# Performance work log

Measured on AMD Instinct MI355X. Metric: run time of the kernel, lower is better.

The kernel has to match this reference:

```python
import jax, jax.numpy as jnp
import numpy as np

K_NEIGHBORS = 32
BN_EPS = 1e-5


def setup_inputs() -> dict:
    key = jax.random.key(0)
    ks = jax.random.split(key, 5)
    B, N, C, OUT = 16, 2048, 3, 32
    x = jax.random.normal(ks[0], (B, N, C), dtype=jnp.float32)
    W1 = jax.random.normal(ks[1], (2 * C, 2 * C), dtype=jnp.float32) * 0.3
    b1 = jax.random.normal(ks[2], (2 * C,), dtype=jnp.float32) * 0.05
    W2 = jax.random.normal(ks[3], (2 * C, OUT), dtype=jnp.float32) * 0.3
    b2 = jax.random.normal(ks[4], (OUT,), dtype=jnp.float32) * 0.05
    return {
        "x": x,
        "W1": W1, "b1": b1,
        "gamma1": jnp.ones((2 * C,), jnp.float32), "beta1": jnp.zeros((2 * C,), jnp.float32),
        "W2": W2, "b2": b2,
        "gamma2": jnp.ones((OUT,), jnp.float32), "beta2": jnp.zeros((OUT,), jnp.float32),
    }


def _batchnorm_train(h, gamma, beta):
    # normalize over all axes except the last (channel) axis, biased variance
    axes = tuple(range(h.ndim - 1))
    mean = jnp.mean(h, axis=axes)
    var = jnp.var(h, axis=axes)
    return gamma * (h - mean) * jax.lax.rsqrt(var + BN_EPS) + beta


def reference(x, W1, b1, gamma1, beta1, W2, b2, gamma2, beta2):
    B, N, C = x.shape
    K = min(K_NEIGHBORS, N)
    # brute-force KNN: squared euclidean distances [B,N,N]
    sq = jnp.sum(x * x, axis=-1)
    d = sq[:, :, None] + sq[:, None, :] - 2.0 * jnp.einsum('bnc,bmc->bnm', x, x)
    _, idx = jax.lax.top_k(-d, K)  # [B,N,K] nearest (self first)
    # gather neighbor points: [B,N,K,C]
    knn = jax.vmap(lambda pts, i: pts[i])(x, idx)
    diffs = x[:, :, None, :] - knn
    h = jnp.concatenate([jnp.broadcast_to(x[:, :, None, :], (B, N, K, C)), diffs], axis=-1)  # [B,N,K,2C]
    h = jax.nn.elu(_batchnorm_train(h @ W1 + b1, gamma1, beta1))
    h = jnp.max(h, axis=2)  # max-pool over K neighbors -> [B,N,2C]
    y = jax.nn.elu(_batchnorm_train(h @ W2 + b2, gamma2, beta2))
    return y
```

## Files before the change

kernel.cpp:

```cpp
#include <hip/hip_runtime.h>
#include <math.h>

namespace {
constexpr int NB = 16, NP = 2048, KNN = 32, CH1 = 6, CH2 = 32;
constexpr int QPB = 8;
constexpr int NBLK = NB * NP / QPB;
constexpr float BN_EPS = 1e-5f;

constexpr size_t OFF_S1REP   = 0;
constexpr size_t OFF_STATS2L = 768;
constexpr size_t OFF_SC1     = 1664;
constexpr size_t OFF_P       = 2048;
constexpr size_t OFF_MINQ    = OFF_P + sizeof(float)*NB*NP*CH1;
}

typedef __attribute__((ext_vector_type(2))) float f32x2;

__device__ __forceinline__ f32x2 pk_mul(f32x2 a, f32x2 b) {
  f32x2 d; asm("v_pk_mul_f32 %0, %1, %2" : "=v"(d) : "v"(a), "v"(b)); return d;
}
__device__ __forceinline__ f32x2 pk_add(f32x2 a, f32x2 b) {
  f32x2 d; asm("v_pk_add_f32 %0, %1, %2" : "=v"(d) : "v"(a), "v"(b)); return d;
}

template <int C> __device__ __forceinline__ int dpp0i(int x) {
  return __builtin_amdgcn_update_dpp(0, x, C, 0xf, 0xf, true);
}
template <int C> __device__ __forceinline__ float dpp0f(float x) {
  return __uint_as_float((unsigned)__builtin_amdgcn_update_dpp(
      0, (int)__float_as_uint(x), C, 0xf, 0xf, true));
}
template <int C> __device__ __forceinline__ float dppInff(float x) {
  return __uint_as_float((unsigned)__builtin_amdgcn_update_dpp(
      0x7F800000, (int)__float_as_uint(x), C, 0xf, 0xf, false));
}
__device__ __forceinline__ int wave_isum_bcast(int x) {
  x += dpp0i<0x111>(x); x += dpp0i<0x112>(x); x += dpp0i<0x114>(x);
  x += dpp0i<0x118>(x); x += dpp0i<0x142>(x); x += dpp0i<0x143>(x);
  return __builtin_amdgcn_readlane(x, 63);
}
__device__ __forceinline__ float wave_fsum63(float x) {
  x += dpp0f<0x111>(x); x += dpp0f<0x112>(x); x += dpp0f<0x114>(x);
  x += dpp0f<0x118>(x); x += dpp0f<0x142>(x); x += dpp0f<0x143>(x);
  return x;
}
__device__ __forceinline__ float wave_fmin63(float x) {
  x = fminf(x, dppInff<0x111>(x)); x = fminf(x, dppInff<0x112>(x));
  x = fminf(x, dppInff<0x114>(x)); x = fminf(x, dppInff<0x118>(x));
  x = fminf(x, dppInff<0x142>(x)); x = fminf(x, dppInff<0x143>(x));
  return x;
}

#define BSEL(m, x, y) ((((x)) & (m)) | (((y)) & ~(m)))

__global__ __launch_bounds__(512, 6) void knn_kernel(const float* __restrict__ x,
                                                     const float* __restrict__ W1,
                                                     const float* __restrict__ b1,
                                                     float* __restrict__ pout,
                                                     float* __restrict__ minq,
                                                     double* __restrict__ s1rep) {
  __shared__ float4 XC[512], YC[512], ZC[512], WC[512];
  __shared__ float red[12][QPB];
  const int lane = threadIdx.x & 63;
  const int w    = threadIdx.x >> 6;
  const int qi   = blockIdx.x * QPB + w;
  const int b    = qi >> 11;
  const int n    = qi & (NP - 1);

  const float* xb = x + (size_t)b * NP * 3;
  {
    const int t = threadIdx.x;
    const int g0 = t >> 6, ls = t & 63;
    float xx[4], yy[4], zz[4], ww[4];
#pragma unroll
    for (int k = 0; k < 4; ++k) {
      const float* pp = xb + (g0*256 + k*64 + ls) * 3;
      float a0 = pp[0], a1 = pp[1], a2 = pp[2];
      xx[k] = a0; yy[k] = a1; zz[k] = a2;
      ww[k] = __fadd_rn(__fadd_rn(__fmul_rn(a0,a0), __fmul_rn(a1,a1)), __fmul_rn(a2,a2));
    }
    XC[t] = (float4){xx[0], xx[1], xx[2], xx[3]};
    YC[t] = (float4){yy[0], yy[1], yy[2], yy[3]};
    ZC[t] = (float4){zz[0], zz[1], zz[2], zz[3]};
    WC[t] = (float4){ww[0], ww[1], ww[2], ww[3]};
  }
  __syncthreads();

  const float* Xs = (const float*)XC;
  const float* Ys = (const float*)YC;
  const float* Zs = (const float*)ZC;
  const float* Ws = (const float*)WC;

  const int vq = n >> 6, lq = n & 63;
  const int qidx = (((vq >> 2) << 6) | lq) * 4 + (vq & 3);
  const float qx = Xs[qidx], qy = Ys[qidx], qz = Zs[qidx], qw = Ws[qidx];
  const f32x2 qx2 = {qx,qx}, qy2 = {qy,qy}, qz2 = {qz,qz}, qw2 = {qw,qw};

  unsigned dd[32];
#pragma unroll
  for (int g = 0; g < 8; ++g) {
    const int cs = g*64 + lane;
    float4 X = XC[cs], Y = YC[cs], Z = ZC[cs], Wv = WC[cs];
    f32x2 x01 = {X.x,X.y}, y01 = {Y.x,Y.y}, z01 = {Z.x,Z.y}, w01 = {Wv.x,Wv.y};
    f32x2 x23 = {X.z,X.w}, y23 = {Y.z,Y.w}, z23 = {Z.z,Z.w}, w23 = {Wv.z,Wv.w};
    f32x2 dotA = pk_add(pk_add(pk_mul(qx2,x01), pk_mul(qy2,y01)), pk_mul(qz2,z01));
    f32x2 dotB = pk_add(pk_add(pk_mul(qx2,x23), pk_mul(qy2,y23)), pk_mul(qz2,z23));
    f32x2 ssA = pk_add(qw2, w01), ssB = pk_add(qw2, w23);
    f32x2 dA = pk_add(dotA, dotA), dB = pk_add(dotB, dotB);
    dd[31-(4*g+0)] = __float_as_uint(__fsub_rn(ssA.x, dA.x));
    dd[31-(4*g+1)] = __float_as_uint(__fsub_rn(ssA.y, dA.y));
    dd[31-(4*g+2)] = __float_as_uint(__fsub_rn(ssB.x, dB.x));
    dd[31-(4*g+3)] = __float_as_uint(__fsub_rn(ssB.y, dB.y));
  }

  unsigned h[16], l[16];
#pragma unroll
  for (int g = 0; g < 16; ++g) {
    h[g] = __builtin_amdgcn_perm(dd[g], dd[g+16], 0x07060302u);
    l[g] = __builtin_amdgcn_perm(dd[g], dd[g+16], 0x05040100u);
  }
#pragma unroll
  for (int g = 0; g < 8; ++g) {
    unsigned hi = h[g], lo = h[g+8];
    h[g]   = __builtin_amdgcn_perm(hi, lo, 0x07030501u);
    h[g+8] = __builtin_amdgcn_perm(hi, lo, 0x06020400u);
  }
#pragma unroll
  for (int g = 0; g < 8; ++g) {
    int k = (g >> 2)*8 + (g & 3);
    unsigned A = h[k], B = h[k+4];
    h[k]   = BSEL(0x0F0F0F0Fu, B >> 4, A);
    h[k+4] = BSEL(0xF0F0F0F0u, A << 4, B);
  }
#pragma unroll
  for (int g = 0; g < 8; ++g) {
    int k = (g >> 1)*4 + (g & 1);
    unsigned A = h[k], B = h[k+2];
    h[k]   = BSEL(0x33333333u, B >> 2, A);
    h[k+2] = BSEL(0xCCCCCCCCu, A << 2, B);
  }
#pragma unroll
  for (int g = 0; g < 8; ++g) {
    int k = g*2;
    unsigned A = h[k], B = h[k+1];
    h[k]   = BSEL(0x55555555u, B >> 1, A);
    h[k+1] = BSEL(0xAAAAAAAAu, A << 1, B);
  }

  unsigned alive = 0xFFFFFFFFu, below = 0u;
  int rem = KNN, ca = 2048;
#pragma unroll
  for (int i = 1; i <= 6; ++i) {
    unsigned zeros = BSEL(h[i], 0u, alive);
    int c0 = wave_isum_bcast(__popc(zeros));
    if (c0 >= rem) { alive = zeros; ca = c0; }
    else { rem -= c0; below |= zeros; alive &= h[i]; ca -= c0; }
  }
#pragma unroll
  for (int i = 7; i <= 15; ++i) {
    if (ca != rem) {
      unsigned zeros = BSEL(h[i], 0u, alive);
      int c0 = wave_isum_bcast(__popc(zeros));
      if (c0 >= rem) { alive = zeros; ca = c0; }
      else { rem -= c0; below |= zeros; alive &= h[i]; ca -= c0; }
    }
  }
  unsigned sel;
  if (__builtin_expect(ca == rem, 1)) {
    sel = below | alive;
  } else {
#pragma unroll
    for (int g = 0; g < 8; ++g) {
      unsigned hi = l[g], lo = l[g+8];
      l[g]   = __builtin_amdgcn_perm(hi, lo, 0x07030501u);
      l[g+8] = __builtin_amdgcn_perm(hi, lo, 0x06020400u);
    }
#pragma unroll
    for (int g = 0; g < 8; ++g) {
      int k = (g >> 2)*8 + (g & 3);
      unsigned A = l[k], B = l[k+4];
      l[k]   = BSEL(0x0F0F0F0Fu, B >> 4, A);
      l[k+4] = BSEL(0xF0F0F0F0u, A << 4, B);
    }
#pragma unroll
    for (int g = 0; g < 8; ++g) {
      int k = (g >> 1)*4 + (g & 1);
      unsigned A = l[k], B = l[k+2];
      l[k]   = BSEL(0x33333333u, B >> 2, A);
      l[k+2] = BSEL(0xCCCCCCCCu, A << 2, B);
    }
#pragma unroll
    for (int g = 0; g < 8; ++g) {
      int k = g*2;
      unsigned A = l[k], B = l[k+1];
      l[k]   = BSEL(0x55555555u, B >> 1, A);
      l[k+1] = BSEL(0xAAAAAAAAu, A << 1, B);
    }
#pragma unroll
    for (int i = 0; i < 16; ++i) {
      if (ca != rem) {
        unsigned zeros = BSEL(l[i], 0u, alive);
        int c0 = wave_isum_bcast(__popc(zeros));
        if (c0 >= rem) { alive = zeros; ca = c0; }
        else { rem -= c0; below |= zeros; alive &= l[i]; ca -= c0; }
      }
    }
    sel = below;
    if (ca == rem) {
      sel |= alive;
    } else {
      for (int v = 0; v < 32; ++v) {
        if (rem <= 0) break;
        bool mine = (alive >> v) & 1;
        unsigned long long mb = __ballot(mine);
        int c = __popcll(mb);
        if (c <= rem) { if (mine) sel |= 1u << v; rem -= c; }
        else {
          if (mine && (int)__popcll(mb & ((1ull << lane) - 1)) < rem) sel |= 1u << v;
          rem = 0;
        }
      }
    }
  }

  float w3[CH1], w4[CH1], w5[CH1];
#pragma unroll
  for (int c = 0; c < CH1; ++c) { w3[c]=W1[3*CH1+c]; w4[c]=W1[4*CH1+c]; w5[c]=W1[5*CH1+c]; }
  float sq_[CH1], sqq[CH1], mn[CH1];
#pragma unroll
  for (int c = 0; c < CH1; ++c) { sq_[c] = 0.f; sqq[c] = 0.f; mn[c] = INFINITY; }
  unsigned m = sel;
  while (m) {
    int v = __builtin_ctz(m); m &= m - 1;
    int idx = (((v >> 2) << 6) | lane) * 4 + (v & 3);
    float px_ = Xs[idx], py_ = Ys[idx], pz_ = Zs[idx];
#pragma unroll
    for (int c = 0; c < CH1; ++c) {
      float qv = px_*w3[c] + py_*w4[c] + pz_*w5[c];
      sq_[c] += qv; sqq[c] += qv*qv; mn[c] = fminf(mn[c], qv);
    }
  }

  float pv[CH1];
#pragma unroll
  for (int c = 0; c < CH1; ++c) {
    float qv = qx*w3[c] + qy*w4[c] + qz*w5[c];
    pv[c] = b1[c] + qx*W1[c] + qy*W1[CH1+c] + qz*W1[2*CH1+c] + qv;
  }

#pragma unroll
  for (int c = 0; c < CH1; ++c) {
    float s  = wave_fsum63(sq_[c]);
    float s2 = wave_fsum63(sqq[c]);
    float mm = wave_fmin63(mn[c]);
    if (lane == 63) {
      minq[qi*CH1 + c] = mm;
      red[c][w]       = fmaf(32.f, pv[c], -s);
      red[CH1 + c][w] = fmaf(32.f, pv[c]*pv[c], fmaf(-2.f*pv[c], s, s2));
    }
  }
  if (lane == 0) {
#pragma unroll
    for (int c = 0; c < CH1; ++c) pout[qi*CH1 + c] = pv[c];
  }
  __syncthreads();
  if (threadIdx.x < 12) {
    float s = 0.f;
#pragma unroll
    for (int ww2 = 0; ww2 < QPB; ++ww2) s += red[threadIdx.x][ww2];
    atomicAdd(s1rep + (blockIdx.x & 7) * 12 + threadIdx.x, (double)s);
  }
}

__global__ __launch_bounds__(256) void stage2_kernel(const float* __restrict__ p,
                                                     const float* __restrict__ minq,
                                                     const double* __restrict__ s1rep,
                                                     const float* __restrict__ gamma1,
                                                     const float* __restrict__ beta1,
                                                     float* __restrict__ sc1g,
                                                     double* __restrict__ stats2L) {
  __shared__ double tot1[12];
  __shared__ float sc1s[12];
  __shared__ float acc[4][27];
  const int t = threadIdx.x;
  if (t < 12) {
    double s = 0.0;
#pragma unroll
    for (int r = 0; r < 8; ++r) s += s1rep[r*12 + t];
    tot1[t] = s;
  }
  __syncthreads();
  if (t < CH1) {
    double cnt  = (double)NB * NP * KNN;
    double mean = tot1[t] / cnt;
    double var  = tot1[CH1 + t] / cnt - mean * mean;
    float scale = gamma1[t] / sqrtf((float)var + BN_EPS);
    sc1s[t] = scale; sc1s[CH1 + t] = beta1[t] - (float)mean * scale;
  }
  __syncthreads();
  if (blockIdx.x == 0 && t < 12) sc1g[t] = sc1s[t];

  const int qi = blockIdx.x * 256 + t;
  const int w = t >> 6, lane = t & 63;
  float me[CH1];
#pragma unroll
  for (int c = 0; c < CH1; ++c) {
    float v = fmaf(sc1s[c], p[qi*CH1 + c] - minq[qi*CH1 + c], sc1s[CH1 + c]);
    me[c] = v > 0.f ? v : expm1f(v);
  }
  float vals[27];
#pragma unroll
  for (int c = 0; c < CH1; ++c) vals[c] = me[c];
  {
    int id = 6;
#pragma unroll
    for (int c = 0; c < CH1; ++c)
#pragma unroll
      for (int d = c; d < CH1; ++d) { vals[id] = me[c]*me[d]; ++id; }
  }
#pragma unroll
  for (int k = 0; k < 27; ++k) {
    float s = wave_fsum63(vals[k]);
    if (lane == 63) acc[w][k] = s;
  }
  __syncthreads();
  if (t < 27)
    atomicAdd(stats2L + (blockIdx.x & 3) * 27 + t,
              (double)((acc[0][t] + acc[1][t]) + (acc[2][t] + acc[3][t])));
}

__global__ __launch_bounds__(256) void out_kernel(const float* __restrict__ p,
                                                  const float* __restrict__ minq,
                                                  const float* __restrict__ sc1,
                                                  const float* __restrict__ W2,
                                                  const float* __restrict__ b2,
                                                  const double* __restrict__ stats2L,
                                                  const float* __restrict__ gamma2,
                                                  const float* __restrict__ beta2,
                                                  float* __restrict__ out) {
  __shared__ float m2[27];
  __shared__ float me_lds[8][CH1];
  __shared__ float s2s[CH2], s2h[CH2];
  const int t = threadIdx.x;
  if (t < 27)
    m2[t] = (float)(((stats2L[t] + stats2L[27+t]) + (stats2L[54+t] + stats2L[81+t])));
  const int qbase = blockIdx.x * 8;
  if (t >= 64 && t < 112) {
    int qs = (t - 64) / 6, c = (t - 64) % 6;
    int qi = qbase + qs;
    float v = fmaf(sc1[c], p[qi*CH1 + c] - minq[qi*CH1 + c], sc1[CH1 + c]);
    me_lds[qs][c] = v > 0.f ? v : expm1f(v);
  }
  __syncthreads();
  if (t < CH2) {
    float wv[CH1];
#pragma unroll
    for (int c = 0; c < CH1; ++c) wv[c] = W2[c*CH2 + t];
    float sy = 0.f;
#pragma unroll
    for (int c = 0; c < CH1; ++c) sy = fmaf(wv[c], m2[c], sy);
    float sy2 = 0.f;
    {
      int id = 6;
#pragma unroll
      for (int c = 0; c < CH1; ++c)
#pragma unroll
        for (int d = c; d < CH1; ++d) {
          float coef = (c == d) ? wv[c]*wv[c] : 2.f*wv[c]*wv[d];
          sy2 = fmaf(coef, m2[id], sy2); ++id;
        }
    }
    const double N = (double)NB * NP;
    double bo   = (double)b2[t];
    double mean = ((double)sy + N*bo) / N;
    double Ey2  = ((double)sy2 + 2.0*bo*(double)sy + N*bo*bo) / N;
    double var  = Ey2 - mean*mean;
    float scale = gamma2[t] / sqrtf((float)var + BN_EPS);
    s2s[t] = scale; s2h[t] = beta2[t] - (float)mean * scale;
  }
  __syncthreads();
  const int qs = t >> 5, o = t & 31;
  const int qi = qbase + qs;
  float y = b2[o];
#pragma unroll
  for (int c = 0; c < CH1; ++c) y = fmaf(me_lds[qs][c], W2[c*CH2 + o], y);
  float r = fmaf(s2s[o], y, s2h[o]);
  out[(size_t)qi*CH2 + o] = r > 0.f ? r : expm1f(r);
}

extern "C" void kernel_launch(void* const* d_in, const int* in_sizes, int n_in,
                              void* d_out, int out_size, void* d_ws, size_t ws_size,
                              hipStream_t stream) {
  const float* x      = (const float*)d_in[0];
  const float* W1     = (const float*)d_in[1];
  const float* b1     = (const float*)d_in[2];
  const float* gamma1 = (const float*)d_in[3];
  const float* beta1  = (const float*)d_in[4];
  const float* W2     = (const float*)d_in[5];
  const float* b2     = (const float*)d_in[6];
  const float* gamma2 = (const float*)d_in[7];
  const float* beta2  = (const float*)d_in[8];
  float* out = (float*)d_out;
  char* ws = (char*)d_ws;

  double* s1rep   = (double*)(ws + OFF_S1REP);
  double* stats2L = (double*)(ws + OFF_STATS2L);
  float* sc1  = (float*)(ws + OFF_SC1);
  float* p    = (float*)(ws + OFF_P);
  float* minq = (float*)(ws + OFF_MINQ);

  hipMemsetAsync(ws, 0, 1664, stream);

  knn_kernel   <<<dim3(NBLK),       dim3(512), 0, stream>>>(x, W1, b1, p, minq, s1rep);
  stage2_kernel<<<dim3(NB*NP/256),  dim3(256), 0, stream>>>(p, minq, s1rep, gamma1, beta1,
                                                            sc1, stats2L);
  out_kernel   <<<dim3(NB*NP/8),    dim3(256), 0, stream>>>(p, minq, sc1, W2, b2,
                                                            stats2L, gamma2, beta2, out);
}
```

Baseline: 72.04 us.

## Process two queries per wave in KNN kernel to amortize tile loads

```diff
diff --git a/kernel.cpp b/kernel.cpp
--- a/kernel.cpp
+++ b/kernel.cpp
@@ -3,7 +3,7 @@
 
 namespace {
 constexpr int NB = 16, NP = 2048, KNN = 32, CH1 = 6, CH2 = 32;
-constexpr int QPB = 8;
+constexpr int QPB = 16;
 constexpr int NBLK = NB * NP / QPB;
 constexpr float BN_EPS = 1e-5f;
 
@@ -53,19 +53,69 @@
 
 #define BSEL(m, x, y) ((((x)) & (m)) | (((y)) & ~(m)))
 
-__global__ __launch_bounds__(512, 6) void knn_kernel(const float* __restrict__ x,
+#define RROUND(alive, below, rem, ca, plane)                  \
+  { unsigned z_ = (alive) & ~(plane);                         \
+    int c_ = wave_isum_bcast(__popc(z_));                     \
+    bool t_ = (c_ >= (rem));                                  \
+    below = t_ ? (below) : ((below) | z_);                    \
+    alive = t_ ? z_ : ((alive) & (plane));                    \
+    ca    = t_ ? c_ : (ca) - c_;                              \
+    rem   = t_ ? (rem) : (rem) - c_; }
+
+#define J16_SPLIT(dd, h, l)                                          \
+  _Pragma("unroll") for (int g_ = 0; g_ < 16; ++g_) {                \
+    h[g_] = __builtin_amdgcn_perm(dd[g_], dd[g_+16], 0x07060302u);   \
+    l[g_] = __builtin_amdgcn_perm(dd[g_], dd[g_+16], 0x05040100u); }
+
+#define TR16(a)                                                      \
+  _Pragma("unroll") for (int g_ = 0; g_ < 8; ++g_) {                 \
+    unsigned hi_ = a[g_], lo_ = a[g_+8];                             \
+    a[g_]   = __builtin_amdgcn_perm(hi_, lo_, 0x07030501u);          \
+    a[g_+8] = __builtin_amdgcn_perm(hi_, lo_, 0x06020400u); }        \
+  _Pragma("unroll") for (int g_ = 0; g_ < 8; ++g_) {                 \
+    int k_ = (g_ >> 2)*8 + (g_ & 3);                                 \
+    unsigned A_ = a[k_], B_ = a[k_+4];                               \
+    a[k_]   = BSEL(0x0F0F0F0Fu, B_ >> 4, A_);                        \
+    a[k_+4] = BSEL(0xF0F0F0F0u, A_ << 4, B_); }                      \
+  _Pragma("unroll") for (int g_ = 0; g_ < 8; ++g_) {                 \
+    int k_ = (g_ >> 1)*4 + (g_ & 1);                                 \
+    unsigned A_ = a[k_], B_ = a[k_+2];                               \
+    a[k_]   = BSEL(0x33333333u, B_ >> 2, A_);                        \
+    a[k_+2] = BSEL(0xCCCCCCCCu, A_ << 2, B_); }                      \
+  _Pragma("unroll") for (int g_ = 0; g_ < 8; ++g_) {                 \
+    int k_ = g_*2;                                                   \
+    unsigned A_ = a[k_], B_ = a[k_+1];                               \
+    a[k_]   = BSEL(0x55555555u, B_ >> 1, A_);                        \
+    a[k_+1] = BSEL(0xAAAAAAAAu, A_ << 1, B_); }
+
+#define TIEBREAK(alive, sel, rem)                                    \
+  for (int v_ = 0; v_ < 32; ++v_) {                                  \
+    if ((rem) <= 0) break;                                           \
+    bool mine_ = ((alive) >> v_) & 1;                                \
+    unsigned long long mb_ = __ballot(mine_);                        \
+    int c_ = __popcll(mb_);                                          \
+    if (c_ <= (rem)) { if (mine_) (sel) |= 1u << v_; (rem) -= c_; }  \
+    else {                                                           \
+      if (mine_ && (int)__popcll(mb_ & ((1ull << lane) - 1)) < (rem))\
+        (sel) |= 1u << v_;                                           \
+      (rem) = 0;                                                     \
+    }                                                                \
+  }
+
+__global__ __launch_bounds__(512, 4) void knn_kernel(const float* __restrict__ x,
                                                      const float* __restrict__ W1,
                                                      const float* __restrict__ b1,
                                                      float* __restrict__ pout,
                                                      float* __restrict__ minq,
                                                      double* __restrict__ s1rep) {
   __shared__ float4 XC[512], YC[512], ZC[512], WC[512];
-  __shared__ float red[12][QPB];
+  __shared__ float red[12][8];
   const int lane = threadIdx.x & 63;
   const int w    = threadIdx.x >> 6;
-  const int qi   = blockIdx.x * QPB + w;
-  const int b    = qi >> 11;
-  const int n    = qi & (NP - 1);
+  const int qiA  = blockIdx.x * QPB + w * 2;
+  const int qiB  = qiA + 1;
+  const int b    = qiA >> 11;
+  const int nA   = qiA & (NP - 1), nB = qiB & (NP - 1);
 
   const float* xb = x + (size_t)b * NP * 3;
   {
@@ -91,145 +141,94 @@
   const float* Zs = (const float*)ZC;
   const float* Ws = (const float*)WC;
 
-  const int vq = n >> 6, lq = n & 63;
-  const int qidx = (((vq >> 2) << 6) | lq) * 4 + (vq & 3);
-  const float qx = Xs[qidx], qy = Ys[qidx], qz = Zs[qidx], qw = Ws[qidx];
-  const f32x2 qx2 = {qx,qx}, qy2 = {qy,qy}, qz2 = {qz,qz}, qw2 = {qw,qw};
-
-  unsigned dd[32];
+  const int vqA = nA >> 6, lqA = nA & 63;
+  const int qidxA = (((vqA >> 2) << 6) | lqA) * 4 + (vqA & 3);
+  const float qxA = Xs[qidxA], qyA = Ys[qidxA], qzA = Zs[qidxA], qwA = Ws[qidxA];
+  const int vqB = nB >> 6, lqB = nB & 63;
+  const int qidxB = (((vqB >> 2) << 6) | lqB) * 4 + (vqB & 3);
+  const float qxB = Xs[qidxB], qyB = Ys[qidxB], qzB = Zs[qidxB], qwB = Ws[qidxB];
+  const f32x2 qxA2 = {qxA,qxA}, qyA2 = {qyA,qyA}, qzA2 = {qzA,qzA}, qwA2 = {qwA,qwA};
+  const f32x2 qxB2 = {qxB,qxB}, qyB2 = {qyB,qyB}, qzB2 = {qzB,qzB}, qwB2 = {qwB,qwB};
+
+  unsigned dA[32], dB[32];
 #pragma unroll
   for (int g = 0; g < 8; ++g) {
     const int cs = g*64 + lane;
     float4 X = XC[cs], Y = YC[cs], Z = ZC[cs], Wv = WC[cs];
     f32x2 x01 = {X.x,X.y}, y01 = {Y.x,Y.y}, z01 = {Z.x,Z.y}, w01 = {Wv.x,Wv.y};
     f32x2 x23 = {X.z,X.w}, y23 = {Y.z,Y.w}, z23 = {Z.z,Z.w}, w23 = {Wv.z,Wv.w};
-    f32x2 dotA = pk_add(pk_add(pk_mul(qx2,x01), pk_mul(qy2,y01)), pk_mul(qz2,z01));
-    f32x2 dotB = pk_add(pk_add(pk_mul(qx2,x23), pk_mul(qy2,y23)), pk_mul(qz2,z23));
-    f32x2 ssA = pk_add(qw2, w01), ssB = pk_add(qw2, w23);
-    f32x2 dA = pk_add(dotA, dotA), dB = pk_add(dotB, dotB);
-    dd[31-(4*g+0)] = __float_as_uint(__fsub_rn(ssA.x, dA.x));
-    dd[31-(4*g+1)] = __float_as_uint(__fsub_rn(ssA.y, dA.y));
-    dd[31-(4*g+2)] = __float_as_uint(__fsub_rn(ssB.x, dB.x));
-    dd[31-(4*g+3)] = __float_as_uint(__fsub_rn(ssB.y, dB.y));
-  }
-
-  unsigned h[16], l[16];
-#pragma unroll
-  for (int g = 0; g < 16; ++g) {
-    h[g] = __builtin_amdgcn_perm(dd[g], dd[g+16], 0x07060302u);
-    l[g] = __builtin_amdgcn_perm(dd[g], dd[g+16], 0x05040100u);
-  }
-#pragma unroll
-  for (int g = 0; g < 8; ++g) {
-    unsigned hi = h[g], lo = h[g+8];
-    h[g]   = __builtin_amdgcn_perm(hi, lo, 0x07030501u);
-    h[g+8] = __builtin_amdgcn_perm(hi, lo, 0x06020400u);
-  }
-#pragma unroll
-  for (int g = 0; g < 8; ++g) {
-    int k = (g >> 2)*8 + (g & 3);
-    unsigned A = h[k], B = h[k+4];
-    h[k]   = BSEL(0x0F0F0F0Fu, B >> 4, A);
-    h[k+4] = BSEL(0xF0F0F0F0u, A << 4, B);
-  }
-#pragma unroll
-  for (int g = 0; g < 8; ++g) {
-    int k = (g >> 1)*4 + (g & 1);
-    unsigned A = h[k], B = h[k+2];
-    h[k]   = BSEL(0x33333333u, B >> 2, A);
-    h[k+2] = BSEL(0xCCCCCCCCu, A << 2, B);
-  }
-#pragma unroll
-  for (int g = 0; g < 8; ++g) {
-    int k = g*2;
-    unsigned A = h[k], B = h[k+1];
-    h[k]   = BSEL(0x55555555u, B >> 1, A);
-    h[k+1] = BSEL(0xAAAAAAAAu, A << 1, B);
-  }
-
-  unsigned alive = 0xFFFFFFFFu, below = 0u;
-  int rem = KNN, ca = 2048;
-#pragma unroll
-  for (int i = 1; i <= 6; ++i) {
-    unsigned zeros = BSEL(h[i], 0u, alive);
-    int c0 = wave_isum_bcast(__popc(zeros));
-    if (c0 >= rem) { alive = zeros; ca = c0; }
-    else { rem -= c0; below |= zeros; alive &= h[i]; ca -= c0; }
-  }
-#pragma unroll
-  for (int i = 7; i <= 15; ++i) {
-    if (ca != rem) {
-      unsigned zeros = BSEL(h[i], 0u, alive);
-      int c0 = wave_isum_bcast(__popc(zeros));
-      if (c0 >= rem) { alive = zeros; ca = c0; }
-      else { rem -= c0; below |= zeros; alive &= h[i]; ca -= c0; }
-    }
-  }
-  unsigned sel;
-  if (__builtin_expect(ca == rem, 1)) {
-    sel = below | alive;
+    {
+      f32x2 dot0 = pk_add(pk_add(pk_mul(qxA2,x01), pk_mul(qyA2,y01)), pk_mul(qzA2,z01));
+      f32x2 dot1 = pk_add(pk_add(pk_mul(qxA2,x23), pk_mul(qyA2,y23)), pk_mul(qzA2,z23));
+      f32x2 ss0 = pk_add(qwA2, w01), ss1 = pk_add(qwA2, w23);
+      f32x2 dt0 = pk_add(dot0, dot0), dt1 = pk_add(dot1, dot1);
+      dA[31-(4*g+0)] = __float_as_uint(__fsub_rn(ss0.x, dt0.x));
+      dA[31-(4*g+1)] = __float_as_uint(__fsub_rn(ss0.y, dt0.y));
+      dA[31-(4*g+2)] = __float_as_uint(__fsub_rn(ss1.x, dt1.x));
+      dA[31-(4*g+3)] = __float_as_uint(__fsub_rn(ss1.y, dt1.y));
+    }
+    {
+      f32x2 dot0 = pk_add(pk_add(pk_mul(qxB2,x01), pk_mul(qyB2,y01)), pk_mul(qzB2,z01));
+      f32x2 dot1 = pk_add(pk_add(pk_mul(qxB2,x23), pk_mul(qyB2,y23)), pk_mul(qzB2,z23));
+      f32x2 ss0 = pk_add(qwB2, w01), ss1 = pk_add(qwB2, w23);
+      f32x2 dt0 = pk_add(dot0, dot0), dt1 = pk_add(dot1, dot1);
+      dB[31-(4*g+0)] = __float_as_uint(__fsub_rn(ss0.x, dt0.x));
+      dB[31-(4*g+1)] = __float_as_uint(__fsub_rn(ss0.y, dt0.y));
+      dB[31-(4*g+2)] = __float_as_uint(__fsub_rn(ss1.x, dt1.x));
+      dB[31-(4*g+3)] = __float_as_uint(__fsub_rn(ss1.y, dt1.y));
+    }
+  }
+
+  unsigned hA[16], lA[16], hB[16], lB[16];
+  J16_SPLIT(dA, hA, lA);
+  TR16(hA);
+  J16_SPLIT(dB, hB, lB);
+  TR16(hB);
+
+  unsigned aliveA = 0xFFFFFFFFu, belowA = 0u, aliveB = 0xFFFFFFFFu, belowB = 0u;
+  int remA = KNN, caA = 2048, remB = KNN, caB = 2048;
+#pragma unroll
+  for (int i = 1; i <= 7; ++i) {
+    RROUND(aliveA, belowA, remA, caA, hA[i]);
+    RROUND(aliveB, belowB, remB, caB, hB[i]);
+  }
+#pragma unroll
+  for (int i = 8; i <= 15; ++i) {
+    if (caA != remA || caB != remB) {
+      RROUND(aliveA, belowA, remA, caA, hA[i]);
+      RROUND(aliveB, belowB, remB, caB, hB[i]);
+    }
+  }
+  unsigned selA, selB;
+  if (__builtin_expect((caA == remA) && (caB == remB), 1)) {
+    selA = belowA | aliveA;
+    selB = belowB | aliveB;
   } else {
-#pragma unroll
-    for (int g = 0; g < 8; ++g) {
-      unsigned hi = l[g], lo = l[g+8];
-      l[g]   = __builtin_amdgcn_perm(hi, lo, 0x07030501u);
-      l[g+8] = __builtin_amdgcn_perm(hi, lo, 0x06020400u);
-    }
-#pragma unroll
-    for (int g = 0; g < 8; ++g) {
-      int k = (g >> 2)*8 + (g & 3);
-      unsigned A = l[k], B = l[k+4];
-      l[k]   = BSEL(0x0F0F0F0Fu, B >> 4, A);
-      l[k+4] = BSEL(0xF0F0F0F0u, A << 4, B);
-    }
-#pragma unroll
-    for (int g = 0; g < 8; ++g) {
-      int k = (g >> 1)*4 + (g & 1);
-      unsigned A = l[k], B = l[k+2];
-      l[k]   = BSEL(0x33333333u, B >> 2, A);
-      l[k+2] = BSEL(0xCCCCCCCCu, A << 2, B);
-    }
-#pragma unroll
-    for (int g = 0; g < 8; ++g) {
-      int k = g*2;
-      unsigned A = l[k], B = l[k+1];
-      l[k]   = BSEL(0x55555555u, B >> 1, A);
-      l[k+1] = BSEL(0xAAAAAAAAu, A << 1, B);
-    }
+    TR16(lA);
+    TR16(lB);
 #pragma unroll
     for (int i = 0; i < 16; ++i) {
-      if (ca != rem) {
-        unsigned zeros = BSEL(l[i], 0u, alive);
-        int c0 = wave_isum_bcast(__popc(zeros));
-        if (c0 >= rem) { alive = zeros; ca = c0; }
-        else { rem -= c0; below |= zeros; alive &= l[i]; ca -= c0; }
+      if (caA != remA || caB != remB) {
+        RROUND(aliveA, belowA, remA, caA, lA[i]);
+        RROUND(aliveB, belowB, remB, caB, lB[i]);
       }
     }
-    sel = below;
-    if (ca == rem) {
-      sel |= alive;
-    } else {
-      for (int v = 0; v < 32; ++v) {
-        if (rem <= 0) break;
-        bool mine = (alive >> v) & 1;
-        unsigned long long mb = __ballot(mine);
-        int c = __popcll(mb);
-        if (c <= rem) { if (mine) sel |= 1u << v; rem -= c; }
-        else {
-          if (mine && (int)__popcll(mb & ((1ull << lane) - 1)) < rem) sel |= 1u << v;
-          rem = 0;
-        }
-      }
-    }
+    selA = belowA;
+    if (caA == remA) selA |= aliveA; else { TIEBREAK(aliveA, selA, remA); }
+    selB = belowB;
+    if (caB == remB) selB |= aliveB; else { TIEBREAK(aliveB, selB, remB); }
   }
 
   float w3[CH1], w4[CH1], w5[CH1];
 #pragma unroll
   for (int c = 0; c < CH1; ++c) { w3[c]=W1[3*CH1+c]; w4[c]=W1[4*CH1+c]; w5[c]=W1[5*CH1+c]; }
-  float sq_[CH1], sqq[CH1], mn[CH1];
-#pragma unroll
-  for (int c = 0; c < CH1; ++c) { sq_[c] = 0.f; sqq[c] = 0.f; mn[c] = INFINITY; }
-  unsigned m = sel;
+  float sqA[CH1], sqqA[CH1], mnA[CH1], sqB[CH1], sqqB[CH1], mnB[CH1];
+#pragma unroll
+  for (int c = 0; c < CH1; ++c) {
+    sqA[c] = 0.f; sqqA[c] = 0.f; mnA[c] = INFINITY;
+    sqB[c] = 0.f; sqqB[c] = 0.f; mnB[c] = INFINITY;
+  }
+  unsigned m = selA;
   while (m) {
     int v = __builtin_ctz(m); m &= m - 1;
     int idx = (((v >> 2) << 6) | lane) * 4 + (v & 3);
@@ -237,37 +236,61 @@
 #pragma unroll
     for (int c = 0; c < CH1; ++c) {
       float qv = px_*w3[c] + py_*w4[c] + pz_*w5[c];
-      sq_[c] += qv; sqq[c] += qv*qv; mn[c] = fminf(mn[c], qv);
-    }
-  }
-
-  float pv[CH1];
+      sqA[c] += qv; sqqA[c] += qv*qv; mnA[c] = fminf(mnA[c], qv);
+    }
+  }
+  m = selB;
+  while (m) {
+    int v = __builtin_ctz(m); m &= m - 1;
+    int idx = (((v >> 2) << 6) | lane) * 4 + (v & 3);
+    float px_ = Xs[idx], py_ = Ys[idx], pz_ = Zs[idx];
+#pragma unroll
+    for (int c = 0; c < CH1; ++c) {
+      float qv = px_*w3[c] + py_*w4[c] + pz_*w5[c];
+      sqB[c] += qv; sqqB[c] += qv*qv; mnB[c] = fminf(mnB[c], qv);
+    }
+  }
+
+  float pvA[CH1], pvB[CH1];
 #pragma unroll
   for (int c = 0; c < CH1; ++c) {
-    float qv = qx*w3[c] + qy*w4[c] + qz*w5[c];
-    pv[c] = b1[c] + qx*W1[c] + qy*W1[CH1+c] + qz*W1[2*CH1+c] + qv;
+    float qvA = qxA*w3[c] + qyA*w4[c] + qzA*w5[c];
+    pvA[c] = b1[c] + qxA*W1[c] + qyA*W1[CH1+c] + qzA*W1[2*CH1+c] + qvA;
+    float qvB = qxB*w3[c] + qyB*w4[c] + qzB*w5[c];
+    pvB[c] = b1[c] + qxB*W1[c] + qyB*W1[CH1+c] + qzB*W1[2*CH1+c] + qvB;
   }
 
 #pragma unroll
   for (int c = 0; c < CH1; ++c) {
-    float s  = wave_fsum63(sq_[c]);
-    float s2 = wave_fsum63(sqq[c]);
-    float mm = wave_fmin63(mn[c]);
+    float sA  = wave_fsum63(sqA[c]);
+    float s2A = wave_fsum63(sqqA[c]);
+    float mmA = wave_fmin63(mnA[c]);
+    float sB  = wave_fsum63(sqB[c]);
+    float s2B = wave_fsum63(sqqB[c]);
+    float mmB = wave_fmin63(mnB[c]);
     if (lane == 63) {
-      minq[qi*CH1 + c] = mm;
-      red[c][w]       = fmaf(32.f, pv[c], -s);
-      red[CH1 + c][w] = fmaf(32.f, pv[c]*pv[c], fmaf(-2.f*pv[c], s, s2));
+      minq[qiA*CH1 + c] = mmA;
+      minq[qiB*CH1 + c] = mmB;
+      float hsA = fmaf(32.f, pvA[c], -sA);
+      float hqA = fmaf(32.f, pvA[c]*pvA[c], fmaf(-2.f*pvA[c], sA, s2A));
+      float hsB = fmaf(32.f, pvB[c], -sB);
+      float hqB = fmaf(32.f, pvB[c]*pvB[c], fmaf(-2.f*pvB[c], sB, s2B));
+      red[c][w]       = hsA + hsB;
+      red[CH1 + c][w] = hqA + hqB;
     }
   }
   if (lane == 0) {
 #pragma unroll
-    for (int c = 0; c < CH1; ++c) pout[qi*CH1 + c] = pv[c];
+    for (int c = 0; c < CH1; ++c) {
+      pout[qiA*CH1 + c] = pvA[c];
+      pout[qiB*CH1 + c] = pvB[c];
+    }
   }
   __syncthreads();
   if (threadIdx.x < 12) {
     float s = 0.f;
 #pragma unroll
-    for (int ww2 = 0; ww2 < QPB; ++ww2) s += red[threadIdx.x][ww2];
+    for (int ww2 = 0; ww2 < 8; ++ww2) s += red[threadIdx.x][ww2];
     atomicAdd(s1rep + (blockIdx.x & 7) * 12 + threadIdx.x, (double)s);
   }
 }
```

Result: slower. 82.32 us (+14.3%).
